# Kernel tuning notes

Hardware: AMD Instinct MI355X
Metric: run time of the kernel (lower is better)

Reference implementation:

```python
import jax, jax.numpy as jnp
import numpy as np

B, H, M, DH = 8, 32, 8, 64  # batch, spatial h=w, heads, dim_head
C = M * DH
HW = H * H


def _make_pos_idx(h: int) -> np.ndarray:
    # A[i, j] = j - i, matching tf.constant([range(i, i+h) for i in range(0, -h, -1)])
    A = np.arange(h)[None, :] - np.arange(h)[:, None]
    horiz = np.tile(A, (h, h))                              # (h^2, h^2)
    vert = np.repeat(np.repeat(A, h, axis=0), h, axis=1)    # (h^2, h^2)
    return (2 * h - 1) * (vert + h - 1) + (horiz + h - 1)   # values in [0, (2h-1)^2)


def setup_inputs() -> dict:
    key = jax.random.key(0)
    ks = jax.random.split(key, 4)
    x = jax.random.normal(ks[0], (B, H, H, C), dtype=jnp.float32)
    w_qkv = jax.random.normal(ks[1], (DH, 3 * DH), dtype=jnp.float32) * (1.0 / np.sqrt(DH))
    b_qkv = jnp.zeros((3 * DH,), dtype=jnp.float32)
    w_ht = jax.random.normal(ks[2], (C, C), dtype=jnp.float32) * (1.0 / np.sqrt(C))
    b_ht = jnp.zeros((C,), dtype=jnp.float32)
    # Glorot-normal scalar table over (2h-1)^2 relative positions
    n_rel = (2 * H - 1) ** 2
    pos_table = jax.random.normal(ks[3], (n_rel,), dtype=jnp.float32) * np.float32(np.sqrt(2.0 / (n_rel + 1)))
    pos_idx = jnp.asarray(_make_pos_idx(H), dtype=jnp.int32)  # (HW, HW)
    return {"x": x, "w_qkv": w_qkv, "b_qkv": b_qkv, "w_ht": w_ht, "b_ht": b_ht,
            "pos_table": pos_table, "pos_idx": pos_idx}


def reference(x, w_qkv, b_qkv, w_ht, b_ht, pos_table, pos_idx):
    b, h, w, c = x.shape
    d_h = c // M
    # split heads into the batch dim: (b*M, h, w, d_h)
    xh = x.reshape(b, h, w, M, d_h).transpose(0, 3, 1, 2, 4).reshape(b * M, h, w, d_h)
    # 1x1 conv == per-pixel dense
    qkv = xh @ w_qkv + b_qkv                       # (b*M, h, w, 3*DH)
    qkv = qkv.reshape(b * M, h * w, DH, 3)
    q, k, v = qkv[..., 0], qkv[..., 1], qkv[..., 2]
    q = q / jnp.sqrt(jnp.float32(DH))
    att = jnp.einsum('bic,bjc->bij', q, k)         # (b*M, HW, HW)
    pos_emb = pos_table[pos_idx]                   # (HW, HW) gathered bias
    att = jax.nn.softmax(att + pos_emb, axis=-1)
    o = jnp.einsum('bij,bjc->bic', att, v)         # (b*M, HW, DH)
    o = o.reshape(b, M, h, w, d_h).transpose(0, 2, 3, 1, 4).reshape(b, h, w, c)
    out = o @ w_ht + b_ht                          # 1x1 head_transform conv
    return (out, att, pos_emb)
```

## Files before the change

### kernel.cpp

```cpp
#include <hip/hip_runtime.h>
#include <hip/hip_bf16.h>

typedef __attribute__((ext_vector_type(8))) __bf16 bf16x8;
typedef __attribute__((ext_vector_type(8))) short  s16x8;
typedef __attribute__((ext_vector_type(4))) short  s16x4;
typedef __attribute__((ext_vector_type(4))) float  f32x4;

#define HW2 1024
#define CDIM 512

static __device__ __forceinline__ unsigned short f2b(float f) {
  __hip_bfloat16 h = __float2bfloat16(f);
  return __builtin_bit_cast(unsigned short, h);
}

static __device__ __forceinline__ f32x4 mfma16(s16x8 a, s16x8 b, f32x4 c) {
  return __builtin_amdgcn_mfma_f32_16x16x32_bf16(
      __builtin_bit_cast(bf16x8, a), __builtin_bit_cast(bf16x8, b), c, 0, 0, 0);
}

__global__ __launch_bounds__(256) void k_prep(
    const float* __restrict__ w_qkv, const float* __restrict__ w_ht,
    const float* __restrict__ table, const int* __restrict__ idx,
    unsigned short* __restrict__ Wtq, unsigned short* __restrict__ Wtk,
    unsigned short* __restrict__ Wtv, unsigned short* __restrict__ WhtT,
    float* __restrict__ pe) {
  int blk = blockIdx.x;
  if (blk < 16) {
    int i = blk * 256 + threadIdx.x;
    int c = i >> 6, k = i & 63;
    const float* src = w_qkv + k * 192 + 3 * c;
    Wtq[i] = f2b(src[0] * 0.125f);
    Wtk[i] = f2b(src[1]);
    Wtv[i] = f2b(src[2]);
  } else if (blk < 1040) {
    int i = (blk - 16) * 256 + threadIdx.x;
    int c = i >> 9, k = i & 511;
    WhtT[i] = f2b(w_ht[k * 512 + c]);
  } else {
    int i = (blk - 1040) * 256 + threadIdx.x;
    #pragma unroll
    for (int j = 0; j < 4; ++j) {
      int p = i + j * 262144;
      pe[p] = table[idx[p]];
    }
  }
}

__global__ __launch_bounds__(256) void k_qkv(const float* __restrict__ x,
    const float* __restrict__ b_qkv,
    const unsigned short* __restrict__ Wtq, const unsigned short* __restrict__ Wtk,
    const unsigned short* __restrict__ Wtv,
    unsigned short* __restrict__ Qb, unsigned short* __restrict__ Kb,
    unsigned short* __restrict__ Vt) {
  int bm = blockIdx.x >> 4;
  int pt = blockIdx.x & 15;
  int wid = threadIdx.x >> 6, lane = threadIdx.x & 63;
  int l15 = lane & 15, lg = lane >> 4;
  int b = bm >> 3, m = bm & 7;
  int pbase = pt * 64 + wid * 16;

  __shared__ unsigned short T[64][200];

  int pA = pbase + l15;
  const float* xp = x + (size_t)(b * HW2 + pA) * CDIM + m * 64 + lg * 8;
  f32x4 xv0 = *(const f32x4*)(xp);
  f32x4 xv1 = *(const f32x4*)(xp + 4);
  f32x4 xv2 = *(const f32x4*)(xp + 32);
  f32x4 xv3 = *(const f32x4*)(xp + 36);
  s16x8 a0, a1;
  #pragma unroll
  for (int j = 0; j < 4; ++j) {
    a0[j]     = (short)f2b(xv0[j]);
    a0[4 + j] = (short)f2b(xv1[j]);
    a1[j]     = (short)f2b(xv2[j]);
    a1[4 + j] = (short)f2b(xv3[j]);
  }

  f32x4 acc[12];
  #pragma unroll
  for (int ct = 0; ct < 12; ++ct) acc[ct] = (f32x4){0.f, 0.f, 0.f, 0.f};

  #pragma unroll
  for (int ct = 0; ct < 12; ++ct) {
    const unsigned short* W = (ct < 4) ? Wtq : (ct < 8 ? Wtk : Wtv);
    int c = (ct & 3) * 16 + l15;
    const unsigned short* wp = W + c * 64 + lg * 8;
    s16x8 b0 = *(const s16x8*)(wp);
    s16x8 b1 = *(const s16x8*)(wp + 32);
    acc[ct] = mfma16(a0, b0, acc[ct]);
    acc[ct] = mfma16(a1, b1, acc[ct]);
  }

  int lrow = wid * 16 + lg * 4;
  #pragma unroll
  for (int ct = 0; ct < 12; ++ct) {
    int s = ct >> 2;
    int c = (ct & 3) * 16 + l15;
    float bias = b_qkv[3 * c + s];
    if (s == 0) bias *= 0.125f;
    #pragma unroll
    for (int i = 0; i < 4; ++i) {
      unsigned short hv = f2b(acc[ct][i] + bias);
      if (s == 0)      T[lrow + i][c] = hv;
      else if (s == 1) T[lrow + i][64 + c] = hv;
      else             T[c][128 + lrow + i] = hv;
    }
  }
  __syncthreads();

  int t = threadIdx.x;
  int r = t >> 2, cp = t & 3;
  size_t prow = (size_t)(bm * HW2 + pt * 64 + r) * 64 + cp * 16;
  *(s16x8*)(Qb + prow)     = *(const s16x8*)&T[r][cp * 16];
  *(s16x8*)(Qb + prow + 8) = *(const s16x8*)&T[r][cp * 16 + 8];
  *(s16x8*)(Kb + prow)     = *(const s16x8*)&T[r][64 + cp * 16];
  *(s16x8*)(Kb + prow + 8) = *(const s16x8*)&T[r][64 + cp * 16 + 8];
  size_t vrow = ((size_t)bm * 64 + r) * HW2 + pt * 64 + cp * 16;
  *(s16x8*)(Vt + vrow)     = *(const s16x8*)&T[r][128 + cp * 16];
  *(s16x8*)(Vt + vrow + 8) = *(const s16x8*)&T[r][128 + cp * 16 + 8];
}

__global__ __launch_bounds__(256, 4) void k_attn(
    const unsigned short* __restrict__ Qb, const unsigned short* __restrict__ Kb,
    const unsigned short* __restrict__ Vt, const float* __restrict__ ptab,
    float* __restrict__ att, unsigned short* __restrict__ O) {
  int bm = blockIdx.x >> 6;
  int qt = blockIdx.x & 63;
  int wid = threadIdx.x >> 6, lane = threadIdx.x & 63;
  int l15 = lane & 15, lg = lane >> 4;

  __shared__ unsigned short P[16][1032];
  __shared__ float redm[4][16];
  __shared__ float reds[4][16];
  __shared__ unsigned short Osm[16][68];

  const unsigned short* qp = Qb + (size_t)(bm * HW2 + qt * 16 + l15) * 64 + lg * 8;
  s16x8 qa0 = *(const s16x8*)qp;
  s16x8 qa1 = *(const s16x8*)(qp + 32);

  f32x4 acc[16];
  const unsigned short* kbase = Kb + (size_t)bm * HW2 * 64;
  #pragma unroll
  for (int ct = 0; ct < 16; ++ct) {
    int col = wid * 256 + ct * 16 + l15;
    const unsigned short* kp = kbase + (size_t)col * 64 + lg * 8;
    s16x8 kb0 = *(const s16x8*)kp;
    s16x8 kb1 = *(const s16x8*)(kp + 32);
    f32x4 a = (f32x4){0.f, 0.f, 0.f, 0.f};
    a = mfma16(qa0, kb0, a);
    a = mfma16(qa1, kb1, a);
    acc[ct] = a;
  }

  int cbase = 1984 - 63 * (qt >> 1) - ((qt & 1) << 4) - lg * 4;
  float pmax[4] = {-1e30f, -1e30f, -1e30f, -1e30f};
  #pragma unroll
  for (int ct = 0; ct < 16; ++ct) {
    int col = wid * 256 + ct * 16 + l15;
    int t0 = 63 * (col >> 5) + (col & 31) + cbase;
    #pragma unroll
    for (int i = 0; i < 4; ++i) {
      float v = acc[ct][i] + ptab[t0 - i];
      acc[ct][i] = v;
      pmax[i] = fmaxf(pmax[i], v);
    }
  }
  #pragma unroll
  for (int i = 0; i < 4; ++i) {
    #pragma unroll
    for (int mk = 1; mk < 16; mk <<= 1)
      pmax[i] = fmaxf(pmax[i], __shfl_xor(pmax[i], mk));
  }
  if (l15 == 0) {
    #pragma unroll
    for (int i = 0; i < 4; ++i) redm[wid][lg * 4 + i] = pmax[i];
  }
  __syncthreads();
  float mrow[4];
  #pragma unroll
  for (int i = 0; i < 4; ++i) {
    int r = lg * 4 + i;
    mrow[i] = fmaxf(fmaxf(redm[0][r], redm[1][r]), fmaxf(redm[2][r], redm[3][r]));
  }

  float psum[4] = {0.f, 0.f, 0.f, 0.f};
  #pragma unroll
  for (int ct = 0; ct < 16; ++ct) {
    #pragma unroll
    for (int i = 0; i < 4; ++i) {
      float e = __expf(acc[ct][i] - mrow[i]);
      acc[ct][i] = e;
      psum[i] += e;
    }
  }
  #pragma unroll
  for (int i = 0; i < 4; ++i) {
    #pragma unroll
    for (int mk = 1; mk < 16; mk <<= 1) psum[i] += __shfl_xor(psum[i], mk);
  }
  if (l15 == 0) {
    #pragma unroll
    for (int i = 0; i < 4; ++i) reds[wid][lg * 4 + i] = psum[i];
  }
  __syncthreads();
  float inv[4];
  #pragma unroll
  for (int i = 0; i < 4; ++i) {
    int r = lg * 4 + i;
    inv[i] = 1.0f / (reds[0][r] + reds[1][r] + reds[2][r] + reds[3][r]);
  }

  float* abase = att + (size_t)(bm * HW2 + qt * 16) * HW2;
  #pragma unroll
  for (int ct = 0; ct < 16; ++ct) {
    int col = wid * 256 + ct * 16 + l15;
    #pragma unroll
    for (int i = 0; i < 4; ++i) {
      int rl = lg * 4 + i;
      float v = acc[ct][i] * inv[i];
      abase[(size_t)rl * HW2 + col] = v;
      P[rl][col] = f2b(v);
    }
  }
  __syncthreads();

  f32x4 o = (f32x4){0.f, 0.f, 0.f, 0.f};
  const unsigned short* vbase = Vt + (size_t)(bm * 64 + wid * 16 + l15) * HW2;
  #pragma unroll
  for (int kt = 0; kt < 32; ++kt) {
    s16x8 pa = *(const s16x8*)&P[l15][kt * 32 + lg * 8];
    s16x8 vb = *(const s16x8*)(vbase + kt * 32 + lg * 8);
    o = mfma16(pa, vb, o);
  }

  #pragma unroll
  for (int i = 0; i < 4; ++i) Osm[lg * 4 + i][wid * 16 + l15] = f2b(o[i]);
  __syncthreads();
  int t = threadIdx.x;
  int row = t >> 4, cpo = t & 15;
  unsigned short* dst = O + (size_t)(bm * HW2 + qt * 16 + row) * 64 + cpo * 4;
  *(s16x4*)dst = *(const s16x4*)&Osm[row][cpo * 4];
}

__global__ __launch_bounds__(256) void k_ht(
    const unsigned short* __restrict__ O, const unsigned short* __restrict__ WhtT,
    const float* __restrict__ b_ht, float* __restrict__ out) {
  int rt = blockIdx.x >> 1;
  int ch = blockIdx.x & 1;
  int wid = threadIdx.x >> 6, lane = threadIdx.x & 63;
  int wr = wid >> 1, wc = wid & 1;
  int l15 = lane & 15, lg = lane >> 4;
  int b = (rt * 32) >> 10;
  int p0 = (rt * 32) & 1023;

  __shared__ unsigned short A[32][520];

  int t = threadIdx.x;
  #pragma unroll
  for (int j = 0; j < 8; ++j) {
    int idx = t * 8 + j * 2048;
    int row = idx >> 9;
    int k0 = idx & 511;
    int m = k0 >> 6, kk = k0 & 63;
    const unsigned short* src = O + (size_t)((b * 8 + m) * HW2 + p0 + row) * 64 + kk;
    *(s16x8*)&A[row][k0] = *(const s16x8*)src;
  }
  __syncthreads();

  f32x4 acc[8];
  #pragma unroll
  for (int ct = 0; ct < 8; ++ct) acc[ct] = (f32x4){0.f, 0.f, 0.f, 0.f};

  #pragma unroll
  for (int kt = 0; kt < 16; ++kt) {
    s16x8 a = *(const s16x8*)&A[wr * 16 + l15][kt * 32 + lg * 8];
    #pragma unroll
    for (int ct = 0; ct < 8; ++ct) {
      int col = ch * 256 + wc * 128 + ct * 16 + l15;
      s16x8 bf = *(const s16x8*)(WhtT + (size_t)col * 512 + kt * 32 + lg * 8);
      acc[ct] = mfma16(a, bf, acc[ct]);
    }
  }

  #pragma unroll
  for (int ct = 0; ct < 8; ++ct) {
    int col = ch * 256 + wc * 128 + ct * 16 + l15;
    float bias = b_ht[col];
    #pragma unroll
    for (int i = 0; i < 4; ++i) {
      int rp = rt * 32 + wr * 16 + lg * 4 + i;
      out[(size_t)rp * 512 + col] = acc[ct][i] + bias;
    }
  }
}

extern "C" void kernel_launch(void* const* d_in, const int* in_sizes, int n_in,
                              void* d_out, int out_size, void* d_ws, size_t ws_size,
                              hipStream_t stream) {
  const float* x         = (const float*)d_in[0];
  const float* w_qkv     = (const float*)d_in[1];
  const float* b_qkv     = (const float*)d_in[2];
  const float* w_ht      = (const float*)d_in[3];
  const float* b_ht      = (const float*)d_in[4];
  const float* pos_table = (const float*)d_in[5];
  const int*   pos_idx   = (const int*)d_in[6];

  float* out = (float*)d_out;
  float* att = out + 4194304;
  float* pe  = att + 67108864;

  char* ws = (char*)d_ws;
  unsigned short* Qb   = (unsigned short*)(ws);
  unsigned short* Kb   = (unsigned short*)(ws + (8u  << 20));
  unsigned short* Vt   = (unsigned short*)(ws + (16u << 20));
  unsigned short* O    = (unsigned short*)(ws + (24u << 20));
  unsigned short* Wtq  = (unsigned short*)(ws + (32u << 20));
  unsigned short* Wtk  = Wtq + 4096;
  unsigned short* Wtv  = Wtk + 4096;
  unsigned short* WhtT = (unsigned short*)(ws + (32u << 20) + 65536);

  k_prep<<<2064, 256, 0, stream>>>(w_qkv, w_ht, pos_table, pos_idx,
                                   Wtq, Wtk, Wtv, WhtT, pe);
  k_qkv <<<1024, 256, 0, stream>>>(x, b_qkv, Wtq, Wtk, Wtv, Qb, Kb, Vt);
  k_attn<<<4096, 256, 0, stream>>>(Qb, Kb, Vt, pos_table, att, O);
  k_ht  <<<512,  256, 0, stream>>>(O, WhtT, b_ht, out);
}
```

Before: 211.3 us.

## Swap MFMA operands for row-contiguous vector stores and drop LDS staging

```diff
diff --git a/kernel.cpp b/kernel.cpp
--- a/kernel.cpp
+++ b/kernel.cpp
@@ -42,7 +42,7 @@
     #pragma unroll
     for (int j = 0; j < 4; ++j) {
       int p = i + j * 262144;
-      pe[p] = table[idx[p]];
+      __builtin_nontemporal_store(table[idx[p]], pe + p);
     }
   }
 }
@@ -60,8 +60,6 @@
   int b = bm >> 3, m = bm & 7;
   int pbase = pt * 64 + wid * 16;
 
-  __shared__ unsigned short T[64][200];
-
   int pA = pbase + l15;
   const float* xp = x + (size_t)(b * HW2 + pA) * CDIM + m * 64 + lg * 8;
   f32x4 xv0 = *(const f32x4*)(xp);
@@ -88,52 +86,54 @@
     const unsigned short* wp = W + c * 64 + lg * 8;
     s16x8 b0 = *(const s16x8*)(wp);
     s16x8 b1 = *(const s16x8*)(wp + 32);
-    acc[ct] = mfma16(a0, b0, acc[ct]);
-    acc[ct] = mfma16(a1, b1, acc[ct]);
-  }
-
-  int lrow = wid * 16 + lg * 4;
-  #pragma unroll
-  for (int ct = 0; ct < 12; ++ct) {
+    if (ct < 8) {
+      acc[ct] = mfma16(b0, a0, acc[ct]);
+      acc[ct] = mfma16(b1, a1, acc[ct]);
+    } else {
+      acc[ct] = mfma16(a0, b0, acc[ct]);
+      acc[ct] = mfma16(a1, b1, acc[ct]);
+    }
+  }
+
+  #pragma unroll
+  for (int ct = 0; ct < 8; ++ct) {
     int s = ct >> 2;
+    int c0 = (ct & 3) * 16 + lg * 4;
+    unsigned short* D = (s == 0) ? Qb : Kb;
+    s16x4 pk;
+    #pragma unroll
+    for (int i = 0; i < 4; ++i) {
+      float bias = b_qkv[3 * (c0 + i) + s];
+      if (s == 0) bias *= 0.125f;
+      pk[i] = (short)f2b(acc[ct][i] + bias);
+    }
+    *(s16x4*)(D + (size_t)(bm * HW2 + pbase + l15) * 64 + c0) = pk;
+  }
+  #pragma unroll
+  for (int ct = 8; ct < 12; ++ct) {
     int c = (ct & 3) * 16 + l15;
-    float bias = b_qkv[3 * c + s];
-    if (s == 0) bias *= 0.125f;
-    #pragma unroll
-    for (int i = 0; i < 4; ++i) {
-      unsigned short hv = f2b(acc[ct][i] + bias);
-      if (s == 0)      T[lrow + i][c] = hv;
-      else if (s == 1) T[lrow + i][64 + c] = hv;
-      else             T[c][128 + lrow + i] = hv;
-    }
-  }
-  __syncthreads();
-
-  int t = threadIdx.x;
-  int r = t >> 2, cp = t & 3;
-  size_t prow = (size_t)(bm * HW2 + pt * 64 + r) * 64 + cp * 16;
-  *(s16x8*)(Qb + prow)     = *(const s16x8*)&T[r][cp * 16];
-  *(s16x8*)(Qb + prow + 8) = *(const s16x8*)&T[r][cp * 16 + 8];
-  *(s16x8*)(Kb + prow)     = *(const s16x8*)&T[r][64 + cp * 16];
-  *(s16x8*)(Kb + prow + 8) = *(const s16x8*)&T[r][64 + cp * 16 + 8];
-  size_t vrow = ((size_t)bm * 64 + r) * HW2 + pt * 64 + cp * 16;
-  *(s16x8*)(Vt + vrow)     = *(const s16x8*)&T[r][128 + cp * 16];
-  *(s16x8*)(Vt + vrow + 8) = *(const s16x8*)&T[r][128 + cp * 16 + 8];
+    float bias = b_qkv[3 * c + 2];
+    s16x4 pk;
+    #pragma unroll
+    for (int i = 0; i < 4; ++i) pk[i] = (short)f2b(acc[ct][i] + bias);
+    *(s16x4*)(Vt + ((size_t)bm * 64 + c) * HW2 + pbase + lg * 4) = pk;
+  }
 }
 
 __global__ __launch_bounds__(256, 4) void k_attn(
     const unsigned short* __restrict__ Qb, const unsigned short* __restrict__ Kb,
     const unsigned short* __restrict__ Vt, const float* __restrict__ ptab,
     float* __restrict__ att, unsigned short* __restrict__ O) {
-  int bm = blockIdx.x >> 6;
-  int qt = blockIdx.x & 63;
+  int r8 = blockIdx.x & 7;
+  int kk = blockIdx.x >> 3;
+  int qt = kk & 63;
+  int bm = ((kk >> 6) << 3) | r8;
   int wid = threadIdx.x >> 6, lane = threadIdx.x & 63;
   int l15 = lane & 15, lg = lane >> 4;
 
   __shared__ unsigned short P[16][1032];
   __shared__ float redm[4][16];
   __shared__ float reds[4][16];
-  __shared__ unsigned short Osm[16][68];
 
   const unsigned short* qp = Qb + (size_t)(bm * HW2 + qt * 16 + l15) * 64 + lg * 8;
   s16x8 qa0 = *(const s16x8*)qp;
@@ -148,80 +148,61 @@
     s16x8 kb0 = *(const s16x8*)kp;
     s16x8 kb1 = *(const s16x8*)(kp + 32);
     f32x4 a = (f32x4){0.f, 0.f, 0.f, 0.f};
-    a = mfma16(qa0, kb0, a);
-    a = mfma16(qa1, kb1, a);
+    a = mfma16(kb0, qa0, a);
+    a = mfma16(kb1, qa1, a);
     acc[ct] = a;
   }
 
-  int cbase = 1984 - 63 * (qt >> 1) - ((qt & 1) << 4) - lg * 4;
-  float pmax[4] = {-1e30f, -1e30f, -1e30f, -1e30f};
+  int cb = 1984 - 63 * (qt >> 1) - ((qt & 1) << 4) - l15;
+  float pm = -1e30f;
   #pragma unroll
   for (int ct = 0; ct < 16; ++ct) {
-    int col = wid * 256 + ct * 16 + l15;
-    int t0 = 63 * (col >> 5) + (col & 31) + cbase;
+    int c0 = wid * 256 + ct * 16 + lg * 4;
+    int t0 = 63 * (c0 >> 5) + (c0 & 31) + cb;
+    f32x4 pv;
+    __builtin_memcpy(&pv, ptab + t0, 16);
     #pragma unroll
     for (int i = 0; i < 4; ++i) {
-      float v = acc[ct][i] + ptab[t0 - i];
+      float v = acc[ct][i] + pv[i];
       acc[ct][i] = v;
-      pmax[i] = fmaxf(pmax[i], v);
-    }
-  }
-  #pragma unroll
-  for (int i = 0; i < 4; ++i) {
-    #pragma unroll
-    for (int mk = 1; mk < 16; mk <<= 1)
-      pmax[i] = fmaxf(pmax[i], __shfl_xor(pmax[i], mk));
-  }
-  if (l15 == 0) {
-    #pragma unroll
-    for (int i = 0; i < 4; ++i) redm[wid][lg * 4 + i] = pmax[i];
-  }
+      pm = fmaxf(pm, v);
+    }
+  }
+  pm = fmaxf(pm, __shfl_xor(pm, 16));
+  pm = fmaxf(pm, __shfl_xor(pm, 32));
+  if (lane < 16) redm[wid][l15] = pm;
   __syncthreads();
-  float mrow[4];
-  #pragma unroll
-  for (int i = 0; i < 4; ++i) {
-    int r = lg * 4 + i;
-    mrow[i] = fmaxf(fmaxf(redm[0][r], redm[1][r]), fmaxf(redm[2][r], redm[3][r]));
-  }
-
-  float psum[4] = {0.f, 0.f, 0.f, 0.f};
+  float mrow = fmaxf(fmaxf(redm[0][l15], redm[1][l15]),
+                     fmaxf(redm[2][l15], redm[3][l15]));
+
+  float ps = 0.f;
   #pragma unroll
   for (int ct = 0; ct < 16; ++ct) {
     #pragma unroll
     for (int i = 0; i < 4; ++i) {
-      float e = __expf(acc[ct][i] - mrow[i]);
+      float e = __expf(acc[ct][i] - mrow);
       acc[ct][i] = e;
-      psum[i] += e;
-    }
-  }
-  #pragma unroll
-  for (int i = 0; i < 4; ++i) {
-    #pragma unroll
-    for (int mk = 1; mk < 16; mk <<= 1) psum[i] += __shfl_xor(psum[i], mk);
-  }
-  if (l15 == 0) {
-    #pragma unroll
-    for (int i = 0; i < 4; ++i) reds[wid][lg * 4 + i] = psum[i];
-  }
+      ps += e;
+    }
+  }
+  ps += __shfl_xor(ps, 16);
+  ps += __shfl_xor(ps, 32);
+  if (lane < 16) reds[wid][l15] = ps;
   __syncthreads();
-  float inv[4];
-  #pragma unroll
-  for (int i = 0; i < 4; ++i) {
-    int r = lg * 4 + i;
-    inv[i] = 1.0f / (reds[0][r] + reds[1][r] + reds[2][r] + reds[3][r]);
-  }
-
-  float* abase = att + (size_t)(bm * HW2 + qt * 16) * HW2;
+  float inv = 1.0f / (reds[0][l15] + reds[1][l15] + reds[2][l15] + reds[3][l15]);
+
+  float* abase = att + (size_t)(bm * HW2 + qt * 16 + l15) * HW2;
   #pragma unroll
   for (int ct = 0; ct < 16; ++ct) {
-    int col = wid * 256 + ct * 16 + l15;
-    #pragma unroll
-    for (int i = 0; i < 4; ++i) {
-      int rl = lg * 4 + i;
-      float v = acc[ct][i] * inv[i];
-      abase[(size_t)rl * HW2 + col] = v;
-      P[rl][col] = f2b(v);
-    }
+    int c0 = wid * 256 + ct * 16 + lg * 4;
+    f32x4 vv;
+    #pragma unroll
+    for (int i = 0; i < 4; ++i) vv[i] = acc[ct][i] * inv;
+    __builtin_nontemporal_store(vv, (f32x4*)(abase + c0));
+    s16x4 pk;
+    #pragma unroll
+    for (int i = 0; i < 4; ++i) pk[i] = (short)f2b(vv[i]);
+    *(s16x4*)&P[l15][c0] = pk;
   }
   __syncthreads();
 
@@ -229,18 +210,14 @@
   const unsigned short* vbase = Vt + (size_t)(bm * 64 + wid * 16 + l15) * HW2;
   #pragma unroll
   for (int kt = 0; kt < 32; ++kt) {
+    s16x8 vb = *(const s16x8*)(vbase + kt * 32 + lg * 8);
     s16x8 pa = *(const s16x8*)&P[l15][kt * 32 + lg * 8];
-    s16x8 vb = *(const s16x8*)(vbase + kt * 32 + lg * 8);
-    o = mfma16(pa, vb, o);
-  }
-
-  #pragma unroll
-  for (int i = 0; i < 4; ++i) Osm[lg * 4 + i][wid * 16 + l15] = f2b(o[i]);
-  __syncthreads();
-  int t = threadIdx.x;
-  int row = t >> 4, cpo = t & 15;
-  unsigned short* dst = O + (size_t)(bm * HW2 + qt * 16 + row) * 64 + cpo * 4;
-  *(s16x4*)dst = *(const s16x4*)&Osm[row][cpo * 4];
+    o = mfma16(vb, pa, o);
+  }
+  s16x4 ok;
+  #pragma unroll
+  for (int i = 0; i < 4; ++i) ok[i] = (short)f2b(o[i]);
+  *(s16x4*)(O + (size_t)(bm * HW2 + qt * 16 + l15) * 64 + wid * 16 + lg * 4) = ok;
 }
 
 __global__ __launch_bounds__(256) void k_ht(
@@ -279,19 +256,19 @@
     for (int ct = 0; ct < 8; ++ct) {
       int col = ch * 256 + wc * 128 + ct * 16 + l15;
       s16x8 bf = *(const s16x8*)(WhtT + (size_t)col * 512 + kt * 32 + lg * 8);
-      acc[ct] = mfma16(a, bf, acc[ct]);
-    }
-  }
-
+      acc[ct] = mfma16(bf, a, acc[ct]);
+    }
+  }
+
+  int rp = rt * 32 + wr * 16 + l15;
   #pragma unroll
   for (int ct = 0; ct < 8; ++ct) {
-    int col = ch * 256 + wc * 128 + ct * 16 + l15;
-    float bias = b_ht[col];
-    #pragma unroll
-    for (int i = 0; i < 4; ++i) {
-      int rp = rt * 32 + wr * 16 + lg * 4 + i;
-      out[(size_t)rp * 512 + col] = acc[ct][i] + bias;
-    }
+    int c0 = ch * 256 + wc * 128 + ct * 16 + lg * 4;
+    f32x4 bb = *(const f32x4*)(b_ht + c0);
+    f32x4 ov;
+    #pragma unroll
+    for (int i = 0; i < 4; ++i) ov[i] = acc[ct][i] + bb[i];
+    __builtin_nontemporal_store(ov, (f32x4*)(out + (size_t)rp * 512 + c0));
   }
 }
 
```

Result: slower. 215.8 us (+2.2%).
